# Optimization experiments

Measured on AMD Instinct MI355X. Metric: run time of the kernel, lower is better.

## Reference

```python
import jax, jax.numpy as jnp
import numpy as np

SEQ_LEN = 8192
HIDDEN = 4096

def setup_inputs() -> dict:
    key = jax.random.key(0)
    k1, k2 = jax.random.split(key)
    hidden = jax.random.normal(k1, (HIDDEN,), dtype=jnp.float32)
    encoder_outputs = jax.random.normal(k2, (SEQ_LEN, 1, HIDDEN), dtype=jnp.float32)
    return {"hidden": hidden, "encoder_outputs": encoder_outputs}

def reference(hidden, encoder_outputs):
    # encoder_outputs: [S, 1, H] -> [S, H]
    enc = encoder_outputs.squeeze(1)
    # energies[i] = dot(hidden, enc[i])  (one batched GEMV instead of a per-step loop)
    energies = enc @ hidden  # [S]
    attn = jax.nn.softmax(energies, axis=0)  # [S]
    # output = enc^T @ attn  (torch.mm(enc.T, attn.unsqueeze(1)).squeeze(1))
    output = enc.T @ attn  # [H]
    return output, attn[:, None]
```

## Files before the change

### kernel.cpp

```cpp
#include <hip/hip_runtime.h>
#include <math.h>

#define S_LEN 8192
#define HDIM  4096
#define H4    1024
#define ABLK  256
#define AGRID 256
#define AWPB  4
#define NWAVES (AGRID * AWPB)
#define RPW   (S_LEN / NWAVES)
#define CBLK  128
#define FB_ATTN 8

__device__ __forceinline__ float wave_reduce_sum(float x) {
#pragma unroll
  for (int o = 32; o > 0; o >>= 1) x += __shfl_xor(x, o, 64);
  return x;
}
__device__ __forceinline__ float wave_reduce_max(float x) {
#pragma unroll
  for (int o = 32; o > 0; o >>= 1) x = fmaxf(x, __shfl_xor(x, o, 64));
  return x;
}

__global__ __launch_bounds__(ABLK) void wavegemv_k(
    const float* __restrict__ enc, const float* __restrict__ hidden,
    float* __restrict__ energies, float* __restrict__ mw, float* __restrict__ lw,
    float* __restrict__ opart) {
  const int t = threadIdx.x;
  const int lane = t & 63;
  const int wid = t >> 6;

  __shared__ float4 hs[H4];
  {
    const float4* hv = (const float4*)hidden;
#pragma unroll
    for (int k = 0; k < 4; ++k) hs[t + k * ABLK] = hv[t + k * ABLK];
  }
  __syncthreads();

  const int gw = blockIdx.x * AWPB + wid;
  const int r0 = gw * RPW;

  float4 acc[16];
#pragma unroll
  for (int k = 0; k < 16; ++k) acc[k] = make_float4(0.f, 0.f, 0.f, 0.f);
  float m = -INFINITY, l = 0.f;

  const float4* encv = (const float4*)enc;
  for (int r = r0; r < r0 + RPW; ++r) {
    const float4* rp = encv + (size_t)r * H4 + lane;
    float4 v[16];
#pragma unroll
    for (int k = 0; k < 16; ++k) v[k] = rp[k * 64];
    float d = 0.f;
#pragma unroll
    for (int k = 0; k < 16; ++k) {
      const float4 h = hs[lane + k * 64];
      d = fmaf(v[k].x, h.x, d);
      d = fmaf(v[k].y, h.y, d);
      d = fmaf(v[k].z, h.z, d);
      d = fmaf(v[k].w, h.w, d);
    }
    d = wave_reduce_sum(d);
    if (lane == 0) energies[r] = d;
    if (d > m) {
      const float sc = __expf(m - d);
      l *= sc;
#pragma unroll
      for (int k = 0; k < 16; ++k) {
        acc[k].x *= sc; acc[k].y *= sc; acc[k].z *= sc; acc[k].w *= sc;
      }
      m = d;
    }
    const float w = __expf(d - m);
    l += w;
#pragma unroll
    for (int k = 0; k < 16; ++k) {
      acc[k].x = fmaf(w, v[k].x, acc[k].x);
      acc[k].y = fmaf(w, v[k].y, acc[k].y);
      acc[k].z = fmaf(w, v[k].z, acc[k].z);
      acc[k].w = fmaf(w, v[k].w, acc[k].w);
    }
  }

  float4* op = (float4*)(opart + (size_t)gw * HDIM);
#pragma unroll
  for (int k = 0; k < 16; ++k) op[lane + k * 64] = acc[k];
  if (lane == 0) { mw[gw] = m; lw[gw] = l; }
}

__global__ __launch_bounds__(256) void finalize_k(
    const float* __restrict__ opart, const float* __restrict__ mw,
    const float* __restrict__ lw, const float* __restrict__ energies,
    float* __restrict__ out) {
  const int t = threadIdx.x;
  const int b = blockIdx.x;
  const int wid = t >> 6;
  const bool lane0 = (t & 63) == 0;

  __shared__ float wg[NWAVES];
  __shared__ float smax[4], ssum[4];

  float mv = -INFINITY;
  for (int g = t; g < NWAVES; g += 256) mv = fmaxf(mv, mw[g]);
  mv = wave_reduce_max(mv);
  if (lane0) smax[wid] = mv;
  __syncthreads();
  const float gm = fmaxf(fmaxf(smax[0], smax[1]), fmaxf(smax[2], smax[3]));

  float lv = 0.f;
  for (int g = t; g < NWAVES; g += 256) lv += lw[g] * __expf(mw[g] - gm);
  lv = wave_reduce_sum(lv);
  if (lane0) ssum[wid] = lv;
  __syncthreads();
  const float invL = 1.f / (ssum[0] + ssum[1] + ssum[2] + ssum[3]);

  for (int g = t; g < NWAVES; g += 256) wg[g] = __expf(mw[g] - gm) * invL;
  __syncthreads();

  if (b < CBLK) {
    const int c  = b * 8 + (t & 7);
    const int g0 = t >> 3;
    float4 acc = {0.f, 0.f, 0.f, 0.f};
    for (int g = g0; g < NWAVES; g += 32) {
      const float w = wg[g];
      const float4 v = ((const float4*)opart)[(size_t)g * H4 + c];
      acc.x = fmaf(w, v.x, acc.x);
      acc.y = fmaf(w, v.y, acc.y);
      acc.z = fmaf(w, v.z, acc.z);
      acc.w = fmaf(w, v.w, acc.w);
    }
    __shared__ float4 sred[256];
    sred[t] = acc;
    __syncthreads();
    if (t < 8) {
      float4 s = sred[t];
#pragma unroll
      for (int q = 1; q < 32; ++q) {
        const float4 v = sred[q * 8 + t];
        s.x += v.x; s.y += v.y; s.z += v.z; s.w += v.w;
      }
      ((float4*)out)[b * 8 + t] = s;
    }
  } else {
    const int i4 = (b - CBLK) * 256 + t;
    const float4 e = ((const float4*)energies)[i4];
    float4 a;
    a.x = __expf(e.x - gm) * invL;
    a.y = __expf(e.y - gm) * invL;
    a.z = __expf(e.z - gm) * invL;
    a.w = __expf(e.w - gm) * invL;
    ((float4*)(out + HDIM))[i4] = a;
  }
}

extern "C" void kernel_launch(void* const* d_in, const int* in_sizes, int n_in,
                              void* d_out, int out_size, void* d_ws, size_t ws_size,
                              hipStream_t stream) {
  const float* hidden = (const float*)d_in[0];
  const float* enc    = (const float*)d_in[1];
  float* out = (float*)d_out;
  float* wsf = (float*)d_ws;

  float* energies = wsf;
  float* mw       = wsf + 8192;
  float* lw       = wsf + 8192 + 1024;
  float* opart    = wsf + 8192 + 2048;

  wavegemv_k<<<AGRID, ABLK, 0, stream>>>(enc, hidden, energies, mw, lw, opart);
  finalize_k<<<CBLK + FB_ATTN, 256, 0, stream>>>(opart, mw, lw, energies, out);
}
```

Baseline: 209.5 us.

## Merge per-wave softmax partials in LDS and double the attention grid

Each block now merges its four waves' online-softmax partial accumulators in shared memory, rescaling by the block max, so only one 16KB partial per block goes to global memory instead of one per wave. The grid doubles to 512 blocks, halving rows per wave to add parallelism. This also halves the partial data the finalize kernel must read. The cost is an extra LDS buffer (64KB) per block, which may limit occupancy, and extra block-level syncs.

Measured after the change: 203.8 us. 1.03x faster.

```diff
diff --git a/kernel.cpp b/kernel.cpp
--- a/kernel.cpp
+++ b/kernel.cpp
@@ -5,10 +5,11 @@
 #define HDIM  4096
 #define H4    1024
 #define ABLK  256
-#define AGRID 256
+#define AGRID 512
 #define AWPB  4
-#define NWAVES (AGRID * AWPB)
-#define RPW   (S_LEN / NWAVES)
+#define NWTOT (AGRID * AWPB)
+#define RPW   (S_LEN / NWTOT)
+#define NPART AGRID
 #define CBLK  128
 #define FB_ATTN 8
 
@@ -25,13 +26,16 @@
 
 __global__ __launch_bounds__(ABLK) void wavegemv_k(
     const float* __restrict__ enc, const float* __restrict__ hidden,
-    float* __restrict__ energies, float* __restrict__ mw, float* __restrict__ lw,
+    float* __restrict__ energies, float* __restrict__ mb, float* __restrict__ lb,
     float* __restrict__ opart) {
   const int t = threadIdx.x;
   const int lane = t & 63;
   const int wid = t >> 6;
 
-  __shared__ float4 hs[H4];
+  __shared__ float4 lds[4 * H4];
+  __shared__ float sm[AWPB], sl[AWPB];
+
+  float4* hs = lds;
   {
     const float4* hv = (const float4*)hidden;
 #pragma unroll
@@ -84,46 +88,72 @@
     }
   }
 
-  float4* op = (float4*)(opart + (size_t)gw * HDIM);
-#pragma unroll
-  for (int k = 0; k < 16; ++k) op[lane + k * 64] = acc[k];
-  if (lane == 0) { mw[gw] = m; lw[gw] = l; }
+  __syncthreads();
+#pragma unroll
+  for (int k = 0; k < 16; ++k) lds[wid * H4 + lane + k * 64] = acc[k];
+  if (lane == 0) { sm[wid] = m; sl[wid] = l; }
+  __syncthreads();
+
+  const float M = fmaxf(fmaxf(sm[0], sm[1]), fmaxf(sm[2], sm[3]));
+  float cw[AWPB];
+#pragma unroll
+  for (int w = 0; w < AWPB; ++w) cw[w] = __expf(sm[w] - M);
+
+  float4* op = (float4*)(opart + (size_t)blockIdx.x * HDIM);
+#pragma unroll
+  for (int p = 0; p < 4; ++p) {
+    const int idx = t + p * ABLK;
+    float4 s = {0.f, 0.f, 0.f, 0.f};
+#pragma unroll
+    for (int w = 0; w < AWPB; ++w) {
+      const float4 v = lds[w * H4 + idx];
+      s.x = fmaf(cw[w], v.x, s.x);
+      s.y = fmaf(cw[w], v.y, s.y);
+      s.z = fmaf(cw[w], v.z, s.z);
+      s.w = fmaf(cw[w], v.w, s.w);
+    }
+    op[idx] = s;
+  }
+  if (t == 0) {
+    mb[blockIdx.x] = M;
+    lb[blockIdx.x] = sl[0] * cw[0] + sl[1] * cw[1] + sl[2] * cw[2] + sl[3] * cw[3];
+  }
 }
 
 __global__ __launch_bounds__(256) void finalize_k(
-    const float* __restrict__ opart, const float* __restrict__ mw,
-    const float* __restrict__ lw, const float* __restrict__ energies,
+    const float* __restrict__ opart, const float* __restrict__ mb,
+    const float* __restrict__ lb, const float* __restrict__ energies,
     float* __restrict__ out) {
   const int t = threadIdx.x;
   const int b = blockIdx.x;
   const int wid = t >> 6;
   const bool lane0 = (t & 63) == 0;
 
-  __shared__ float wg[NWAVES];
+  __shared__ float wg[NPART];
   __shared__ float smax[4], ssum[4];
 
   float mv = -INFINITY;
-  for (int g = t; g < NWAVES; g += 256) mv = fmaxf(mv, mw[g]);
+  for (int g = t; g < NPART; g += 256) mv = fmaxf(mv, mb[g]);
   mv = wave_reduce_max(mv);
   if (lane0) smax[wid] = mv;
   __syncthreads();
   const float gm = fmaxf(fmaxf(smax[0], smax[1]), fmaxf(smax[2], smax[3]));
 
   float lv = 0.f;
-  for (int g = t; g < NWAVES; g += 256) lv += lw[g] * __expf(mw[g] - gm);
+  for (int g = t; g < NPART; g += 256) lv += lb[g] * __expf(mb[g] - gm);
   lv = wave_reduce_sum(lv);
   if (lane0) ssum[wid] = lv;
   __syncthreads();
   const float invL = 1.f / (ssum[0] + ssum[1] + ssum[2] + ssum[3]);
 
-  for (int g = t; g < NWAVES; g += 256) wg[g] = __expf(mw[g] - gm) * invL;
+  for (int g = t; g < NPART; g += 256) wg[g] = __expf(mb[g] - gm) * invL;
   __syncthreads();
 
   if (b < CBLK) {
     const int c  = b * 8 + (t & 7);
     const int g0 = t >> 3;
     float4 acc = {0.f, 0.f, 0.f, 0.f};
-    for (int g = g0; g < NWAVES; g += 32) {
+    for (int g = g0; g < NPART; g += 32) {
       const float w = wg[g];
       const float4 v = ((const float4*)opart)[(size_t)g * H4 + c];
       acc.x = fmaf(w, v.x, acc.x);
@@ -164,10 +194,10 @@
   float* wsf = (float*)d_ws;
 
   float* energies = wsf;
-  float* mw       = wsf + 8192;
-  float* lw       = wsf + 8192 + 1024;
-  float* opart    = wsf + 8192 + 2048;
-
-  wavegemv_k<<<AGRID, ABLK, 0, stream>>>(enc, hidden, energies, mw, lw, opart);
-  finalize_k<<<CBLK + FB_ATTN, 256, 0, stream>>>(opart, mw, lw, energies, out);
-}
+  float* mb       = wsf + 8192;
+  float* lb       = wsf + 8192 + 512;
+  float* opart    = wsf + 8192 + 1024;
+
+  wavegemv_k<<<AGRID, ABLK, 0, stream>>>(enc, hidden, energies, mb, lb, opart);
+  finalize_k<<<CBLK + FB_ATTN, 256, 0, stream>>>(opart, mb, lb, energies, out);
+}
```
